# Performance work log

Hardware: AMD Instinct MI355X
Metric: run time of the kernel (lower is better)

## Reference

```python
import jax, jax.numpy as jnp
import numpy as np

TAU = 0.01
RHO = 1.99
SIGMA = 1.0 / TAU / 72.0  # 1/tau/72 as in __init__
N_IT = 10  # n_it_max


def nabla2(x):
    # forward finite differences: channel 0 along W (last axis), channel 1 along H
    u = jnp.zeros(x.shape + (2,), x.dtype)
    u = u.at[..., :, :-1, 0].add(x[..., :, 1:] - x[..., :, :-1])
    u = u.at[..., :-1, :, 1].add(x[..., 1:, :] - x[..., :-1, :])
    return u


def nabla2_adjoint(u):
    x = jnp.zeros(u.shape[:-1], u.dtype)
    x = x.at[..., :, :-1].add(-u[..., :, :-1, 0])
    x = x.at[..., :, 1:].add(u[..., :, :-1, 0])
    x = x.at[..., :-1, :].add(-u[..., :-1, :, 1])
    x = x.at[..., 1:, :].add(u[..., :-1, :, 1])
    return x


def epsilon2(I):
    # Jacobian of the vector field I [..., H, W, 2] -> G [..., H, W, 4]
    I0, I1 = I[..., 0], I[..., 1]
    G = jnp.zeros(I0.shape + (4,), I.dtype)
    G = G.at[..., 0].add(I0)                                  # G0 = I0 - shift_H(I0)
    G = G.at[..., 1:, :, 0].add(-I0[..., :-1, :])
    G = G.at[..., :, 1:, 1].add(I0[..., :, 1:] - I0[..., :, :-1])  # G1: W-diff of I0
    G = G.at[..., 2].add(I1)                                  # G2 = I1 - shift_W(I1)
    G = G.at[..., :, 1:, 2].add(-I1[..., :, :-1])
    G = G.at[..., :-1, :, 3].add(I1[..., 1:, :] - I1[..., :-1, :])  # G3: H-diff of I1
    return G


def epsilon2_adjoint(G):
    I = jnp.zeros(G.shape[:-1] + (2,), G.dtype)
    I = I.at[..., 0].add(G[..., 0])
    I = I.at[..., :-1, :, 0].add(-G[..., 1:, :, 0])
    I = I.at[..., :, :-1, 0].add(-G[..., :, 1:, 1])
    I = I.at[..., :, 1:, 0].add(G[..., :, 1:, 1])
    I = I.at[..., 1].add(G[..., 2])
    I = I.at[..., :, :-1, 1].add(-G[..., :, 1:, 2])
    I = I.at[..., :-1, :, 1].add(-G[..., :-1, :, 3])
    I = I.at[..., 1:, :, 1].add(G[..., :-1, :, 3])
    return I


def setup_inputs() -> dict:
    key = jax.random.key(0)
    y = jax.random.normal(key, (4, 512, 512), dtype=jnp.float32)
    return {"y": y, "ths": 1}


def reference(y, ths):
    lam1 = ths * 0.1
    lam2 = ths * 0.15

    def prox_tau_fr(r):
        left = jnp.sqrt(jnp.sum(r * r, axis=-1)) / (TAU * lam1)
        return r - r / jnp.maximum(left, 1.0)[..., None]

    def prox_sigma_g_conj(u):
        return u / jnp.maximum(jnp.sqrt(jnp.sum(u * u, axis=-1)) / lam2, 1.0)[..., None]

    x2 = y
    r2 = jnp.zeros(y.shape + (2,), y.dtype)
    u2 = jnp.zeros(y.shape + (4,), y.dtype)

    def step(carry, _):
        x2, r2, u2 = carry
        tmp = TAU * epsilon2_adjoint(u2)
        x = (x2 - nabla2_adjoint(tmp) + TAU * y) / (1.0 + TAU)  # prox_tau_fx
        r = prox_tau_fr(r2 + tmp)
        u = prox_sigma_g_conj(
            u2 + SIGMA * epsilon2(nabla2(2.0 * x - x2) - (2.0 * r - r2))
        )
        x2 = x2 + RHO * (x - x2)
        r2 = r2 + RHO * (r - r2)
        u2 = u2 + RHO * (u - u2)
        return (x2, r2, u2), None

    (x2, r2, u2), _ = jax.lax.scan(step, (x2, r2, u2), None, length=N_IT)
    return x2
```

## Files before the change

### kernel.cpp

```cpp
#include <hip/hip_runtime.h>
#include <hip/hip_fp16.h>
#include <math.h>

#define HH 512
#define WW 512
#define BB 4
#define NPIX (BB * HH * WW)

#define HS 4
#define NSX 9
#define NBAND (HH / HS)
#define NWAVES (NSX * NBAND * BB)
#define NBLK (NWAVES / 4)

constexpr float TAUf   = 0.01f;
constexpr float RHOf   = 1.99f;
constexpr float SIGMAf = (float)(1.0 / 0.01 / 72.0);
constexpr float INV1PT = (float)(1.0 / 1.01);

__device__ __forceinline__ float SD(float v) { return __shfl_down(v, 1, 64); }
__device__ __forceinline__ float SUp(float v) { return __shfl_up(v, 1, 64); }


template <int MODE>
__global__ __launch_bounds__(256) void sweep(
    const float* __restrict__ y, const int* __restrict__ ths_p,
    const uint2* __restrict__ f_in, const uint2* __restrict__ u_in,
    uint2* __restrict__ f_out, uint2* __restrict__ u_out,
    float* __restrict__ xout)
{
    const int tid  = threadIdx.x;
    const int lane = tid & 63;
    const int wid  = blockIdx.x * 4 + (tid >> 6);
    const int sx   = wid % NSX;
    const int t2   = wid / NSX;
    const int band = t2 & (NBAND - 1);
    const int b    = t2 / NBAND;
    const int R0   = band * HS;
    const int w    = sx * 60 - 2 + lane;
    const int boff = b * (HH * WW);
    const bool wok = ((unsigned)w) < (unsigned)WW;
    const float mA = (w >= 1 && w < WW) ? 1.f : 0.f;
    const float mB = (w >= 0 && w < WW - 1) ? 1.f : 0.f;
    const bool cok = (lane >= 2) && (lane < 62) && (w < WW);

    const float ths  = (float)ths_p[0];
    const float tl1_ = TAUf * (ths * 0.1f);
    const float l2_  = ths * 0.15f;

    float uf0[4], uf1[4], uf2[4], uf3[4];
    float i0r[2], i1r[2];
    float sr[2];
    float t1r[2];
    float v0r[4];
    float v1r[2];
    #pragma unroll
    for (int q = 0; q < 4; ++q) { uf0[q]=uf1[q]=uf2[q]=uf3[q]=0.f; v0r[q]=0.f; }
    i0r[0]=i0r[1]=i1r[0]=i1r[1]=0.f;
    sr[0]=sr[1]=0.f; t1r[0]=t1r[1]=0.f; v1r[0]=v1r[1]=0.f;

    auto uload = [&](int row) -> uint2 {
        uint2 z; z.x = 0u; z.y = 0u;
        if (((unsigned)row) < (unsigned)HH && wok)
            z = u_in[(size_t)(boff + row * WW + w)];
        return z;
    };
    auto fload = [&](int row) -> uint2 {
        uint2 z; z.x = 0u; z.y = 0u;
        if (((unsigned)row) < (unsigned)HH && wok)
            z = f_in[(size_t)(boff + row * WW + w)];
        return z;
    };
    auto unpk = [&](int slot, uint2 raw) {
        __half2 lo = *(reinterpret_cast<__half2*>(&raw.x));
        __half2 hi = *(reinterpret_cast<__half2*>(&raw.y));
        uf0[slot] = __low2float(lo); uf1[slot] = __high2float(lo);
        uf2[slot] = __low2float(hi); uf3[slot] = __high2float(hi);
    };
    auto compI = [&](int rr, int islot, int c, int d, int uu_) {
        if (((unsigned)rr) < (unsigned)HH) {
            float hD  = (rr < HH - 1) ? 1.f : 0.f;
            float u1c = uf1[c], u2c = uf2[c];
            i0r[islot] = uf0[c] - uf0[d] - SD(u1c) + mA * u1c;
            i1r[islot] = u2c - SD(u2c) - hD * uf3[c] + uf3[uu_];
        } else { i0r[islot] = 0.f; i1r[islot] = 0.f; }
    };

    if (MODE == 2) {
        unpk(2, uload(R0 - 2));
        unpk(3, uload(R0 - 1));
        unpk(0, uload(R0));
        compI(R0 - 1, 1, 3, 0, 2);
        uint2 puA = uload(R0 + 1);
        uint2 puB = uload(R0 + 2);
        uint2 pfA = fload(R0);
        uint2 pfB = fload(R0 + 1);
        #pragma unroll
        for (int k = 0; k < HS; ++k) {
            const int rr = R0 + k;
            unpk((k + 1) & 3, puA);
            puA = puB;
            if (k < HS - 2) puB = uload(R0 + k + 3);
            __half2 lo = *(reinterpret_cast<__half2*>(&pfA.x));
            __half2 hi = *(reinterpret_cast<__half2*>(&pfA.y));
            float x2v = __low2float(lo);
            float yv  = __high2float(hi);
            pfA = pfB;
            if (k < HS - 2) pfB = fload(R0 + k + 2);
            compI(rr, k & 1, k & 3, (k + 1) & 3, (k + 3) & 3);
            float hD = (rr < HH - 1) ? 1.f : 0.f;
            float i0c = i0r[k & 1], i1c = i1r[k & 1], i1u = i1r[(k + 1) & 1];
            float i0l = SUp(i0c);
            float na = TAUf * (mA * i0l - mB * i0c + i1u - hD * i1c);
            float x = (x2v - na + TAUf * yv) * INV1PT;
            if (cok) xout[boff + rr * WW + w] = x2v + RHOf * (x - x2v);
        }
        return;
    }

    auto compS = [&](int rr, int isc, int isp,
                     float yv, float x2v, float r20v, float r21v, unsigned yraw,
                     bool coreRow, float &sOut, float &t0Out, float &t1Out) {
        if (((unsigned)rr) < (unsigned)HH) {
            if (MODE == 0) {
                sOut = yv; t0Out = 0.f; t1Out = 0.f;
                if (coreRow && cok) {
                    int idx = boff + rr * WW + w;
                    unsigned hb = (unsigned)__half_as_ushort(__float2half(yv));
                    uint2 st; st.x = hb; st.y = hb << 16;
                    f_out[(size_t)idx] = st;
                }
            } else {
                float hD = (rr < HH - 1) ? 1.f : 0.f;
                float i0c = i0r[isc], i1c = i1r[isc], i1u = i1r[isp];
                float i0l = SUp(i0c);
                float na = TAUf * (mA * i0l - mB * i0c + i1u - hD * i1c);
                float x = (x2v - na + TAUf * yv) * INV1PT;
                float rr0 = r20v + TAUf * i0c;
                float rr1 = r21v + TAUf * i1c;
                float d = rr0 * rr0 + rr1 * rr1;
                float rinv = fminf(tl1_ * __builtin_amdgcn_rsqf(d), 1.0f);
                float r0 = rr0 - rr0 * rinv;
                float r1 = rr1 - rr1 * rinv;
                sOut  = 2.f * x  - x2v;
                t0Out = 2.f * r0 - r20v;
                t1Out = 2.f * r1 - r21v;
                if (coreRow && cok) {
                    int idx = boff + rr * WW + w;
                    __half2 lo2 = __floats2half2_rn(x2v + RHOf * (x - x2v),
                                                    r20v + RHOf * (r0 - r20v));
                    unsigned r1b = (unsigned)__half_as_ushort(
                        __float2half(r21v + RHOf * (r1 - r21v)));
                    uint2 st; st.x = *(unsigned*)&lo2; st.y = r1b | (yraw << 16);
                    f_out[(size_t)idx] = st;
                }
            }
        } else { sOut = 0.f; t0Out = 0.f; t1Out = 0.f; }
    };

    auto compU = [&](int ro, int v0c_s, int v0u_s, int v1c_s, int v1d_s, int uslot) {
        float hD  = (ro < HH - 1) ? 1.f : 0.f;
        float v0c = v0r[v0c_s], v0u = v0r[v0u_s];
        float v1c = v1r[v1c_s], v1d = v1r[v1d_s];
        float v0l = SUp(v0c);
        float v1l = SUp(v1c);
        float G0 = v0c - v0u;
        float G1 = mA * (v0c - v0l);
        float G2 = v1c - mA * v1l;
        float G3 = hD * (v1d - v1c);
        float u0v, u1v, u2v, u3v;
        if (MODE == 0) { u0v = u1v = u2v = u3v = 0.f; }
        else { u0v = uf0[uslot]; u1v = uf1[uslot]; u2v = uf2[uslot]; u3v = uf3[uslot]; }
        float uu0 = u0v + SIGMAf * G0;
        float uu1 = u1v + SIGMAf * G1;
        float uu2 = u2v + SIGMAf * G2;
        float uu3 = u3v + SIGMAf * G3;
        float d = uu0 * uu0 + uu1 * uu1 + uu2 * uu2 + uu3 * uu3;
        float ui = fminf(l2_ * __builtin_amdgcn_rsqf(d), 1.0f);
        if (cok) {
            int idx = boff + ro * WW + w;
            __half2 lo = __floats2half2_rn(u0v + RHOf * (uu0 * ui - u0v),
                                           u1v + RHOf * (uu1 * ui - u1v));
            __half2 hi = __floats2half2_rn(u2v + RHOf * (uu2 * ui - u2v),
                                           u3v + RHOf * (uu3 * ui - u3v));
            uint2 st; st.x = *(unsigned*)&lo; st.y = *(unsigned*)&hi;
            u_out[(size_t)idx] = st;
        }
    };

    uint2 puA, puB, pfA, pfB;
    puA.x = puA.y = puB.x = puB.y = 0u;
    pfA.x = pfA.y = pfB.x = pfB.y = 0u;
    float pyA = 0.f, pyB = 0.f;
    if (MODE != 0) {
        unpk(1, uload(R0 - 3));
        unpk(2, uload(R0 - 2));
        unpk(3, uload(R0 - 1));
        compI(R0 - 2, 0, 2, 3, 1);
        puA = uload(R0);
        puB = uload(R0 + 1);
        pfA = fload(R0 - 1);
        pfB = fload(R0);
    } else {
        int rowA = R0 - 1; bool okA = (((unsigned)rowA) < (unsigned)HH) && wok;
        pyA = okA ? y[boff + rowA * WW + w] : 0.f;
        pyB = wok ? y[boff + R0 * WW + w] : 0.f;
    }

    #pragma unroll
    for (int k = 0; k < HS + 3; ++k) {
        const int rr = R0 - 1 + k;

        float yv, x2v = 0.f, r20v = 0.f, r21v = 0.f; unsigned yraw = 0u;
        if (MODE != 0) {
            unpk(k & 3, puA);
            puA = puB;
            if (k <= HS) puB = uload(R0 + k + 2);
            __half2 lo = *(reinterpret_cast<__half2*>(&pfA.x));
            __half2 hi = *(reinterpret_cast<__half2*>(&pfA.y));
            x2v  = __low2float(lo);  r20v = __high2float(lo);
            r21v = __low2float(hi);  yv   = __high2float(hi);
            yraw = pfA.y >> 16;
            pfA = pfB;
            if (k <= HS) pfB = fload(R0 + k + 1);
        } else {
            yv = pyA;
            pyA = pyB;
            if (k <= HS) {
                int row = R0 + k + 1;
                bool ok = (((unsigned)row) < (unsigned)HH) && wok;
                pyB = ok ? y[boff + row * WW + w] : 0.f;
            }
        }
        if (MODE != 0) compI(rr, (k + 1) & 1, (k + 3) & 3, k & 3, (k + 2) & 3);

        float sN, t0N, t1N;
        compS(rr, (k + 1) & 1, k & 1, yv, x2v, r20v, r21v, yraw,
              (k >= 1 && k <= HS), sN, t0N, t1N);

        {
            float sPrev  = sr[k & 1];
            float t1Prev = t1r[k & 1];
            float hDm1   = (rr < HH) ? 1.f : 0.f;
            v0r[(k + 3) & 3] = mB * (SD(sN) - sN) - t0N;
            v1r[k & 1]       = hDm1 * (sN - sPrev) - t1Prev;
            sr[(k + 1) & 1]  = sN;
            t1r[(k + 1) & 1] = t1N;
        }

        if (k >= 3) compU(R0 - 3 + k, (k + 1) & 3, k & 3, (k + 1) & 1, k & 1,
                          (k + 1) & 3);
    }
}

extern "C" void kernel_launch(void* const* d_in, const int* in_sizes, int n_in,
                              void* d_out, int out_size, void* d_ws, size_t ws_size,
                              hipStream_t stream)
{
    const float* y   = (const float*)d_in[0];
    const int*   ths = (const int*)d_in[1];
    uint2* ws2 = (uint2*)d_ws;

    uint2* FA = ws2;
    uint2* UA = ws2 + (size_t)NPIX;
    uint2* FB = ws2 + 2 * (size_t)NPIX;
    uint2* UB = ws2 + 3 * (size_t)NPIX;
    float* xout = (float*)d_out;

    dim3 block(256);
    dim3 grid(NBLK);

    sweep<0><<<grid, block, 0, stream>>>(y, ths, nullptr, nullptr, FB, UB, nullptr);
    uint2 *fi = FB, *ui = UB, *fo = FA, *uo = UA;
    for (int it = 1; it <= 8; ++it) {
        sweep<1><<<grid, block, 0, stream>>>(y, ths, fi, ui, fo, uo, nullptr);
        uint2* t;
        t = fi; fi = fo; fo = t;
        t = ui; ui = uo; uo = t;
    }
    sweep<2><<<grid, block, 0, stream>>>(y, ths, fi, ui, nullptr, nullptr, xout);
}
```

Before: 160.2 us.

## Interleave f and u state into one 16-byte record per pixel

Merges the two separate 8-byte state arrays (x2/r2/y packed f and the 4-channel u) into a single uint4 array, so each row is fetched with one 16-byte load and written with one 16-byte store. The f values are kept in a small register ring so they can be stored together with u, which lags by two rows. This halves the number of load and store instructions and address streams per pixel. The cost is more live registers for the ring, and the MODE 2 pass now reads the u half of each record it does not need.

```diff
diff --git a/kernel.cpp b/kernel.cpp
--- a/kernel.cpp
+++ b/kernel.cpp
@@ -25,8 +25,7 @@
 template <int MODE>
 __global__ __launch_bounds__(256) void sweep(
     const float* __restrict__ y, const int* __restrict__ ths_p,
-    const uint2* __restrict__ f_in, const uint2* __restrict__ u_in,
-    uint2* __restrict__ f_out, uint2* __restrict__ u_out,
+    const uint4* __restrict__ s_in, uint4* __restrict__ s_out,
     float* __restrict__ xout)
 {
     const int tid  = threadIdx.x;
@@ -50,30 +49,26 @@
 
     float uf0[4], uf1[4], uf2[4], uf3[4];
     float i0r[2], i1r[2];
-    float sr[2];
-    float t1r[2];
-    float v0r[4];
-    float v1r[2];
+    float sr[2], t1r[2];
+    float v0r[4], v1r[2];
+    uint2 fring[4];
     #pragma unroll
-    for (int q = 0; q < 4; ++q) { uf0[q]=uf1[q]=uf2[q]=uf3[q]=0.f; v0r[q]=0.f; }
+    for (int q = 0; q < 4; ++q) {
+        uf0[q]=uf1[q]=uf2[q]=uf3[q]=0.f; v0r[q]=0.f;
+        fring[q].x = 0u; fring[q].y = 0u;
+    }
     i0r[0]=i0r[1]=i1r[0]=i1r[1]=0.f;
     sr[0]=sr[1]=0.f; t1r[0]=t1r[1]=0.f; v1r[0]=v1r[1]=0.f;
 
-    auto uload = [&](int row) -> uint2 {
-        uint2 z; z.x = 0u; z.y = 0u;
+    auto sload = [&](int row) -> uint4 {
+        uint4 z; z.x = z.y = z.z = z.w = 0u;
         if (((unsigned)row) < (unsigned)HH && wok)
-            z = u_in[(size_t)(boff + row * WW + w)];
+            z = s_in[(size_t)(boff + row * WW + w)];
         return z;
     };
-    auto fload = [&](int row) -> uint2 {
-        uint2 z; z.x = 0u; z.y = 0u;
-        if (((unsigned)row) < (unsigned)HH && wok)
-            z = f_in[(size_t)(boff + row * WW + w)];
-        return z;
-    };
-    auto unpk = [&](int slot, uint2 raw) {
-        __half2 lo = *(reinterpret_cast<__half2*>(&raw.x));
-        __half2 hi = *(reinterpret_cast<__half2*>(&raw.y));
+    auto unpkU = [&](int slot, uint4 rec) {
+        __half2 lo = *(reinterpret_cast<__half2*>(&rec.z));
+        __half2 hi = *(reinterpret_cast<__half2*>(&rec.w));
         uf0[slot] = __low2float(lo); uf1[slot] = __high2float(lo);
         uf2[slot] = __low2float(hi); uf3[slot] = __high2float(hi);
     };
@@ -87,26 +82,25 @@
     };
 
     if (MODE == 2) {
-        unpk(2, uload(R0 - 2));
-        unpk(3, uload(R0 - 1));
-        unpk(0, uload(R0));
+        uint4 rm2 = sload(R0 - 2);
+        uint4 rm1 = sload(R0 - 1);
+        uint4 rc0 = sload(R0);
+        unpkU(2, rm2); unpkU(3, rm1); unpkU(0, rc0);
         compI(R0 - 1, 1, 3, 0, 2);
-        uint2 puA = uload(R0 + 1);
-        uint2 puB = uload(R0 + 2);
-        uint2 pfA = fload(R0);
-        uint2 pfB = fload(R0 + 1);
+        uint4 sF = rc0;
+        uint4 sA = sload(R0 + 1);
+        uint4 sB = sload(R0 + 2);
         #pragma unroll
         for (int k = 0; k < HS; ++k) {
             const int rr = R0 + k;
-            unpk((k + 1) & 3, puA);
-            puA = puB;
-            if (k < HS - 2) puB = uload(R0 + k + 3);
-            __half2 lo = *(reinterpret_cast<__half2*>(&pfA.x));
-            __half2 hi = *(reinterpret_cast<__half2*>(&pfA.y));
+            uint4 nl; nl.x = nl.y = nl.z = nl.w = 0u;
+            if (k < HS - 2) nl = sload(R0 + k + 3);
+            unpkU((k + 1) & 3, sA);
+            __half2 lo = *(reinterpret_cast<__half2*>(&sF.x));
+            __half2 hi = *(reinterpret_cast<__half2*>(&sF.y));
             float x2v = __low2float(lo);
             float yv  = __high2float(hi);
-            pfA = pfB;
-            if (k < HS - 2) pfB = fload(R0 + k + 2);
+            sF = sA; sA = sB; sB = nl;
             compI(rr, k & 1, k & 3, (k + 1) & 3, (k + 3) & 3);
             float hD = (rr < HH - 1) ? 1.f : 0.f;
             float i0c = i0r[k & 1], i1c = i1r[k & 1], i1u = i1r[(k + 1) & 1];
@@ -118,89 +112,18 @@
         return;
     }
 
-    auto compS = [&](int rr, int isc, int isp,
-                     float yv, float x2v, float r20v, float r21v, unsigned yraw,
-                     bool coreRow, float &sOut, float &t0Out, float &t1Out) {
-        if (((unsigned)rr) < (unsigned)HH) {
-            if (MODE == 0) {
-                sOut = yv; t0Out = 0.f; t1Out = 0.f;
-                if (coreRow && cok) {
-                    int idx = boff + rr * WW + w;
-                    unsigned hb = (unsigned)__half_as_ushort(__float2half(yv));
-                    uint2 st; st.x = hb; st.y = hb << 16;
-                    f_out[(size_t)idx] = st;
-                }
-            } else {
-                float hD = (rr < HH - 1) ? 1.f : 0.f;
-                float i0c = i0r[isc], i1c = i1r[isc], i1u = i1r[isp];
-                float i0l = SUp(i0c);
-                float na = TAUf * (mA * i0l - mB * i0c + i1u - hD * i1c);
-                float x = (x2v - na + TAUf * yv) * INV1PT;
-                float rr0 = r20v + TAUf * i0c;
-                float rr1 = r21v + TAUf * i1c;
-                float d = rr0 * rr0 + rr1 * rr1;
-                float rinv = fminf(tl1_ * __builtin_amdgcn_rsqf(d), 1.0f);
-                float r0 = rr0 - rr0 * rinv;
-                float r1 = rr1 - rr1 * rinv;
-                sOut  = 2.f * x  - x2v;
-                t0Out = 2.f * r0 - r20v;
-                t1Out = 2.f * r1 - r21v;
-                if (coreRow && cok) {
-                    int idx = boff + rr * WW + w;
-                    __half2 lo2 = __floats2half2_rn(x2v + RHOf * (x - x2v),
-                                                    r20v + RHOf * (r0 - r20v));
-                    unsigned r1b = (unsigned)__half_as_ushort(
-                        __float2half(r21v + RHOf * (r1 - r21v)));
-                    uint2 st; st.x = *(unsigned*)&lo2; st.y = r1b | (yraw << 16);
-                    f_out[(size_t)idx] = st;
-                }
-            }
-        } else { sOut = 0.f; t0Out = 0.f; t1Out = 0.f; }
-    };
-
-    auto compU = [&](int ro, int v0c_s, int v0u_s, int v1c_s, int v1d_s, int uslot) {
-        float hD  = (ro < HH - 1) ? 1.f : 0.f;
-        float v0c = v0r[v0c_s], v0u = v0r[v0u_s];
-        float v1c = v1r[v1c_s], v1d = v1r[v1d_s];
-        float v0l = SUp(v0c);
-        float v1l = SUp(v1c);
-        float G0 = v0c - v0u;
-        float G1 = mA * (v0c - v0l);
-        float G2 = v1c - mA * v1l;
-        float G3 = hD * (v1d - v1c);
-        float u0v, u1v, u2v, u3v;
-        if (MODE == 0) { u0v = u1v = u2v = u3v = 0.f; }
-        else { u0v = uf0[uslot]; u1v = uf1[uslot]; u2v = uf2[uslot]; u3v = uf3[uslot]; }
-        float uu0 = u0v + SIGMAf * G0;
-        float uu1 = u1v + SIGMAf * G1;
-        float uu2 = u2v + SIGMAf * G2;
-        float uu3 = u3v + SIGMAf * G3;
-        float d = uu0 * uu0 + uu1 * uu1 + uu2 * uu2 + uu3 * uu3;
-        float ui = fminf(l2_ * __builtin_amdgcn_rsqf(d), 1.0f);
-        if (cok) {
-            int idx = boff + ro * WW + w;
-            __half2 lo = __floats2half2_rn(u0v + RHOf * (uu0 * ui - u0v),
-                                           u1v + RHOf * (uu1 * ui - u1v));
-            __half2 hi = __floats2half2_rn(u2v + RHOf * (uu2 * ui - u2v),
-                                           u3v + RHOf * (uu3 * ui - u3v));
-            uint2 st; st.x = *(unsigned*)&lo; st.y = *(unsigned*)&hi;
-            u_out[(size_t)idx] = st;
-        }
-    };
-
-    uint2 puA, puB, pfA, pfB;
-    puA.x = puA.y = puB.x = puB.y = 0u;
-    pfA.x = pfA.y = pfB.x = pfB.y = 0u;
+    uint4 sF, sA, sB;
+    sF.x=sF.y=sF.z=sF.w=0u; sA=sF; sB=sF;
     float pyA = 0.f, pyB = 0.f;
     if (MODE != 0) {
-        unpk(1, uload(R0 - 3));
-        unpk(2, uload(R0 - 2));
-        unpk(3, uload(R0 - 1));
+        uint4 a = sload(R0 - 3);
+        uint4 c = sload(R0 - 2);
+        uint4 d = sload(R0 - 1);
+        unpkU(1, a); unpkU(2, c); unpkU(3, d);
         compI(R0 - 2, 0, 2, 3, 1);
-        puA = uload(R0);
-        puB = uload(R0 + 1);
-        pfA = fload(R0 - 1);
-        pfB = fload(R0);
+        sF = d;
+        sA = sload(R0);
+        sB = sload(R0 + 1);
     } else {
         int rowA = R0 - 1; bool okA = (((unsigned)rowA) < (unsigned)HH) && wok;
         pyA = okA ? y[boff + rowA * WW + w] : 0.f;
@@ -213,16 +136,15 @@
 
         float yv, x2v = 0.f, r20v = 0.f, r21v = 0.f; unsigned yraw = 0u;
         if (MODE != 0) {
-            unpk(k & 3, puA);
-            puA = puB;
-            if (k <= HS) puB = uload(R0 + k + 2);
-            __half2 lo = *(reinterpret_cast<__half2*>(&pfA.x));
-            __half2 hi = *(reinterpret_cast<__half2*>(&pfA.y));
+            uint4 nl; nl.x = nl.y = nl.z = nl.w = 0u;
+            if (k <= HS) nl = sload(R0 + k + 2);
+            unpkU(k & 3, sA);
+            __half2 lo = *(reinterpret_cast<__half2*>(&sF.x));
+            __half2 hi = *(reinterpret_cast<__half2*>(&sF.y));
             x2v  = __low2float(lo);  r20v = __high2float(lo);
             r21v = __low2float(hi);  yv   = __high2float(hi);
-            yraw = pfA.y >> 16;
-            pfA = pfB;
-            if (k <= HS) pfB = fload(R0 + k + 1);
+            yraw = sF.y >> 16;
+            sF = sA; sA = sB; sB = nl;
         } else {
             yv = pyA;
             pyA = pyB;
@@ -235,8 +157,43 @@
         if (MODE != 0) compI(rr, (k + 1) & 1, (k + 3) & 3, k & 3, (k + 2) & 3);
 
         float sN, t0N, t1N;
-        compS(rr, (k + 1) & 1, k & 1, yv, x2v, r20v, r21v, yraw,
-              (k >= 1 && k <= HS), sN, t0N, t1N);
+        {
+            const bool coreRow = (k >= 1 && k <= HS);
+            if (((unsigned)rr) < (unsigned)HH) {
+                if (MODE == 0) {
+                    sN = yv; t0N = 0.f; t1N = 0.f;
+                    if (coreRow) {
+                        unsigned hb = (unsigned)__half_as_ushort(__float2half(yv));
+                        fring[(k + 1) & 3].x = hb;
+                        fring[(k + 1) & 3].y = hb << 16;
+                    }
+                } else {
+                    float hD = (rr < HH - 1) ? 1.f : 0.f;
+                    float i0c = i0r[(k + 1) & 1], i1c = i1r[(k + 1) & 1];
+                    float i1u = i1r[k & 1];
+                    float i0l = SUp(i0c);
+                    float na = TAUf * (mA * i0l - mB * i0c + i1u - hD * i1c);
+                    float x = (x2v - na + TAUf * yv) * INV1PT;
+                    float rr0 = r20v + TAUf * i0c;
+                    float rr1 = r21v + TAUf * i1c;
+                    float dd = rr0 * rr0 + rr1 * rr1;
+                    float rinv = fminf(tl1_ * __builtin_amdgcn_rsqf(dd), 1.0f);
+                    float r0 = rr0 - rr0 * rinv;
+                    float r1 = rr1 - rr1 * rinv;
+                    sN  = 2.f * x  - x2v;
+                    t0N = 2.f * r0 - r20v;
+                    t1N = 2.f * r1 - r21v;
+                    if (coreRow) {
+                        __half2 lo2 = __floats2half2_rn(x2v + RHOf * (x - x2v),
+                                                        r20v + RHOf * (r0 - r20v));
+                        unsigned r1b = (unsigned)__half_as_ushort(
+                            __float2half(r21v + RHOf * (r1 - r21v)));
+                        fring[(k + 1) & 3].x = *(unsigned*)&lo2;
+                        fring[(k + 1) & 3].y = r1b | (yraw << 16);
+                    }
+                }
+            } else { sN = 0.f; t0N = 0.f; t1N = 0.f; }
+        }
 
         {
             float sPrev  = sr[k & 1];
@@ -248,8 +205,43 @@
             t1r[(k + 1) & 1] = t1N;
         }
 
-        if (k >= 3) compU(R0 - 3 + k, (k + 1) & 3, k & 3, (k + 1) & 1, k & 1,
-                          (k + 1) & 3);
+        if (k >= 3) {
+            const int ro = R0 - 3 + k;
+            float hD  = (ro < HH - 1) ? 1.f : 0.f;
+            float v0c = v0r[(k + 1) & 3], v0u = v0r[k & 3];
+            float v1c = v1r[(k + 1) & 1], v1d = v1r[k & 1];
+            float v0l = SUp(v0c);
+            float v1l = SUp(v1c);
+            float G0 = v0c - v0u;
+            float G1 = mA * (v0c - v0l);
+            float G2 = v1c - mA * v1l;
+            float G3 = hD * (v1d - v1c);
+            float u0v, u1v, u2v, u3v;
+            if (MODE == 0) { u0v = u1v = u2v = u3v = 0.f; }
+            else {
+                const int us = (k + 1) & 3;
+                u0v = uf0[us]; u1v = uf1[us]; u2v = uf2[us]; u3v = uf3[us];
+            }
+            float uu0 = u0v + SIGMAf * G0;
+            float uu1 = u1v + SIGMAf * G1;
+            float uu2 = u2v + SIGMAf * G2;
+            float uu3 = u3v + SIGMAf * G3;
+            float dd = uu0 * uu0 + uu1 * uu1 + uu2 * uu2 + uu3 * uu3;
+            float uiS = fminf(l2_ * __builtin_amdgcn_rsqf(dd), 1.0f);
+            if (cok) {
+                int idx = boff + ro * WW + w;
+                __half2 lo = __floats2half2_rn(u0v + RHOf * (uu0 * uiS - u0v),
+                                               u1v + RHOf * (uu1 * uiS - u1v));
+                __half2 hi = __floats2half2_rn(u2v + RHOf * (uu2 * uiS - u2v),
+                                               u3v + RHOf * (uu3 * uiS - u3v));
+                uint4 st;
+                st.x = fring[(k + 3) & 3].x;
+                st.y = fring[(k + 3) & 3].y;
+                st.z = *(unsigned*)&lo;
+                st.w = *(unsigned*)&hi;
+                s_out[(size_t)idx] = st;
+            }
+        }
     }
 }
 
@@ -259,24 +251,18 @@
 {
     const float* y   = (const float*)d_in[0];
     const int*   ths = (const int*)d_in[1];
-    uint2* ws2 = (uint2*)d_ws;
-
-    uint2* FA = ws2;
-    uint2* UA = ws2 + (size_t)NPIX;
-    uint2* FB = ws2 + 2 * (size_t)NPIX;
-    uint2* UB = ws2 + 3 * (size_t)NPIX;
+    uint4* SA = (uint4*)d_ws;
+    uint4* SB = SA + (size_t)NPIX;
     float* xout = (float*)d_out;
 
     dim3 block(256);
     dim3 grid(NBLK);
 
-    sweep<0><<<grid, block, 0, stream>>>(y, ths, nullptr, nullptr, FB, UB, nullptr);
-    uint2 *fi = FB, *ui = UB, *fo = FA, *uo = UA;
+    sweep<0><<<grid, block, 0, stream>>>(y, ths, nullptr, SB, nullptr);
+    uint4 *si = SB, *so = SA;
     for (int it = 1; it <= 8; ++it) {
-        sweep<1><<<grid, block, 0, stream>>>(y, ths, fi, ui, fo, uo, nullptr);
-        uint2* t;
-        t = fi; fi = fo; fo = t;
-        t = ui; ui = uo; uo = t;
-    }
-    sweep<2><<<grid, block, 0, stream>>>(y, ths, fi, ui, nullptr, nullptr, xout);
+        sweep<1><<<grid, block, 0, stream>>>(y, ths, si, so, nullptr);
+        uint4* t = si; si = so; so = t;
+    }
+    sweep<2><<<grid, block, 0, stream>>>(y, ths, si, nullptr, xout);
 }
```

New measurement: 164.3 us. +2.5%, slower.
